# Kernel optimization log

Hardware: AMD Instinct MI355X
Metric: run time of the kernel (lower is better)

The kernel has to match this reference:

```python
import jax, jax.numpy as jnp
import numpy as np

B, T, D, H = 4, 2048, 1024, 16
HS = D // H

def _layernorm(x, g, b, eps=1e-5):
    mu = jnp.mean(x, axis=-1, keepdims=True)
    var = jnp.var(x, axis=-1, keepdims=True)
    return (x - mu) * jax.lax.rsqrt(var + eps) * g + b

def setup_inputs() -> dict:
    key = jax.random.key(0)
    ks = jax.random.split(key, 8)
    s = 0.02
    return {
        "x": jax.random.normal(ks[0], (B, T, D), jnp.float32),
        "wq": jax.random.normal(ks[1], (D, D), jnp.float32) * s,
        "wk": jax.random.normal(ks[2], (D, D), jnp.float32) * s,
        "wv": jax.random.normal(ks[3], (D, D), jnp.float32) * s,
        "wo": jax.random.normal(ks[4], (D, D), jnp.float32) * s,
        "bo": jnp.zeros((D,), jnp.float32),
        "w1": jax.random.normal(ks[5], (D, 4 * D), jnp.float32) * s,
        "b1": jnp.zeros((4 * D,), jnp.float32),
        "w2": jax.random.normal(ks[6], (4 * D, D), jnp.float32) * s,
        "b2": jnp.zeros((D,), jnp.float32),
        "g1": jnp.ones((D,), jnp.float32),
        "be1": jnp.zeros((D,), jnp.float32),
        "g2": jnp.ones((D,), jnp.float32),
        "be2": jnp.zeros((D,), jnp.float32),
    }

def reference(x, wq, wk, wv, wo, bo, w1, b1, w2, b2, g1, be1, g2, be2):
    b, t, d = x.shape
    h = H
    hs = d // h
    # --- pre-LN + multi-head causal self-attention ---
    xn = _layernorm(x, g1, be1)
    q = (xn @ wq).reshape(b, t, h, hs).transpose(0, 2, 1, 3)  # [b,h,t,hs]
    k = (xn @ wk).reshape(b, t, h, hs).transpose(0, 2, 1, 3)
    v = (xn @ wv).reshape(b, t, h, hs).transpose(0, 2, 1, 3)
    # NOTE: original scales by C**-0.5 where C = embedded_size (not head_size)
    scale = jnp.asarray(d, x.dtype) ** -0.5
    wei = jnp.einsum("bhqd,bhkd->bhqk", q, k) * scale
    causal = jnp.tril(jnp.ones((t, t), bool))
    wei = jnp.where(causal, wei, -jnp.inf)
    wei = jax.nn.softmax(wei, axis=-1)
    attn = jnp.einsum("bhqk,bhkd->bhqd", wei, v)
    attn = attn.transpose(0, 2, 1, 3).reshape(b, t, d)
    x = x + attn @ wo + bo
    # --- pre-LN + FFN ---
    xn2 = _layernorm(x, g2, be2)
    x = x + jax.nn.relu(xn2 @ w1 + b1) @ w2 + b2
    return x
```

## Files before the change

### kernel.cpp

```cpp
#include <hip/hip_runtime.h>
#include <hip/hip_bf16.h>
#include <stdint.h>

typedef __hip_bfloat16 bf16;
typedef __attribute__((ext_vector_type(8))) short bf16x8_t;
typedef __attribute__((ext_vector_type(4))) float f32x4_t;
typedef __attribute__((ext_vector_type(16))) float f32x16_t;
typedef __attribute__((ext_vector_type(2))) unsigned int u32x2_t;

#define B_ 4
#define T_ 2048
#define D_ 1024
#define H_ 16
#define HS_ 64

__device__ __forceinline__ void gload_lds16(const void* g, void* l) {
    __builtin_amdgcn_global_load_lds(
        (const __attribute__((address_space(1))) unsigned int*)g,
        (__attribute__((address_space(3))) unsigned int*)l, 16, 0, 0);
}

__device__ __forceinline__ bf16x8_t ldsv8(const bf16* p) {
    return *(const bf16x8_t*)p;
}

__device__ __forceinline__ unsigned pack2(float a, float b) {
    union { bf16 h[2]; unsigned u; } t;
    t.h[0] = __float2bfloat16(a);
    t.h[1] = __float2bfloat16(b);
    return t.u;
}

__global__ __launch_bounds__(256) void transpose_cvt(
    const float* __restrict__ W, bf16* __restrict__ WT, int K, int N)
{
    __shared__ float tile[32][33];
    const int nbx = N >> 5;
    const int bx = blockIdx.x % nbx;
    const int by = blockIdx.x / nbx;
    const int n0 = bx << 5, k0 = by << 5;
    const int tx = threadIdx.x & 31, ty = threadIdx.x >> 5;
#pragma unroll
    for (int i = 0; i < 32; i += 8)
        tile[ty + i][tx] = W[(long)(k0 + ty + i) * N + n0 + tx];
    __syncthreads();
#pragma unroll
    for (int i = 0; i < 32; i += 8)
        WT[(long)(n0 + ty + i) * K + k0 + tx] = __float2bfloat16(tile[tx][ty + i]);
}

__global__ __launch_bounds__(256) void vhead_transpose(
    const bf16* __restrict__ V, bf16* __restrict__ VT)
{
    __shared__ bf16 tile[32][33];
    int idx = blockIdx.x;
    const int tt  = idx & 63;   idx >>= 6;
    const int hst = idx & 1;    idx >>= 1;
    const int bh  = idx;
    const int b = bh >> 4, h = bh & 15;
    const int tx = threadIdx.x & 31, ty = threadIdx.x >> 5;
    const long vrow = (long)b * T_ + tt * 32;
    const int  vcol = h * HS_ + hst * 32;
#pragma unroll
    for (int i = 0; i < 32; i += 8)
        tile[ty + i][tx] = V[(vrow + ty + i) * D_ + vcol + tx];
    __syncthreads();
    const long orow = (long)bh * HS_ + hst * 32;
#pragma unroll
    for (int i = 0; i < 32; i += 8)
        VT[(orow + ty + i) * T_ + tt * 32 + tx] = tile[tx][ty + i];
}

__global__ __launch_bounds__(256) void ln_k(
    const float* __restrict__ x, const float* __restrict__ g,
    const float* __restrict__ be, bf16* __restrict__ out)
{
    const long row = blockIdx.x;
    const int t = threadIdx.x;
    const float4 v = ((const float4*)(x + row * D_))[t];
    float s  = v.x + v.y + v.z + v.w;
    float s2 = v.x * v.x + v.y * v.y + v.z * v.z + v.w * v.w;
#pragma unroll
    for (int m = 1; m < 64; m <<= 1) {
        s  += __shfl_xor(s, m, 64);
        s2 += __shfl_xor(s2, m, 64);
    }
    __shared__ float red[8];
    const int wv = t >> 6, ln = t & 63;
    if (ln == 0) { red[wv] = s; red[4 + wv] = s2; }
    __syncthreads();
    s  = red[0] + red[1] + red[2] + red[3];
    s2 = red[4] + red[5] + red[6] + red[7];
    const float mu  = s * (1.f / (float)D_);
    const float var = s2 * (1.f / (float)D_) - mu * mu;
    const float rs  = rsqrtf(var + 1e-5f);
    const float4 gv = ((const float4*)g)[t];
    const float4 bv = ((const float4*)be)[t];
    union { bf16 h[4]; short4 s4; } u;
    u.h[0] = __float2bfloat16((v.x - mu) * rs * gv.x + bv.x);
    u.h[1] = __float2bfloat16((v.y - mu) * rs * gv.y + bv.y);
    u.h[2] = __float2bfloat16((v.z - mu) * rs * gv.z + bv.z);
    u.h[3] = __float2bfloat16((v.w - mu) * rs * gv.w + bv.w);
    ((short4*)(out + row * D_))[t] = u.s4;
}

template<int HAS_BIAS, int RELU, int HAS_RES, int OUT_BF16>
__global__ __launch_bounds__(256, 2) void gemm_bt(
    const bf16* __restrict__ A, const bf16* __restrict__ BT,
    const float* __restrict__ bias, const float* __restrict__ res,
    void* __restrict__ Cout, int M, int N, int K)
{
    __shared__ bf16 As[128 * 32];
    __shared__ bf16 Bs[128 * 32];
    const int tid  = threadIdx.x;
    const int wave = tid >> 6;
    const int lane = tid & 63;
    const int nbn  = N >> 7;
    const int bm = blockIdx.x / nbn;
    const int bn = blockIdx.x % nbn;
    const int row0 = bm << 7, col0 = bn << 7;
    const int wm = wave & 1, wn = wave >> 1;

    const int srow = tid >> 2;
    const int scol = (tid & 3) << 3;
    const bf16* aSrc = A  + (long)(row0 + srow) * K + scol;
    const bf16* bSrc = BT + (long)(col0 + srow) * K + scol;
    bf16* aDst1 = As + wave * 512;
    bf16* aDst2 = As + 2048 + wave * 512;
    bf16* bDst1 = Bs + wave * 512;
    bf16* bDst2 = Bs + 2048 + wave * 512;

    f32x4_t acc[4][4] = {};

    const int fr = lane & 15;
    const int fk = (lane >> 4) << 3;

    for (int k0 = 0; k0 < K; k0 += 32) {
        gload_lds16(aSrc + k0, aDst1);
        gload_lds16(aSrc + k0 + (long)64 * K, aDst2);
        gload_lds16(bSrc + k0, bDst1);
        gload_lds16(bSrc + k0 + (long)64 * K, bDst2);
        __syncthreads();
        bf16x8_t a[4], b[4];
#pragma unroll
        for (int m = 0; m < 4; ++m)
            a[m] = ldsv8(As + (wm * 64 + m * 16 + fr) * 32 + fk);
#pragma unroll
        for (int n = 0; n < 4; ++n)
            b[n] = ldsv8(Bs + (wn * 64 + n * 16 + fr) * 32 + fk);
#pragma unroll
        for (int m = 0; m < 4; ++m)
#pragma unroll
            for (int n = 0; n < 4; ++n)
                acc[m][n] = __builtin_amdgcn_mfma_f32_16x16x32_bf16(a[m], b[n], acc[m][n], 0, 0, 0);
        __syncthreads();
    }

    const int orow = (lane >> 4) << 2;
#pragma unroll
    for (int m = 0; m < 4; ++m) {
        const int rbase = row0 + wm * 64 + m * 16 + orow;
#pragma unroll
        for (int n = 0; n < 4; ++n) {
            const int c = col0 + wn * 64 + n * 16 + fr;
            float bv = 0.f;
            if (HAS_BIAS) bv = bias[c];
#pragma unroll
            for (int r = 0; r < 4; ++r) {
                float v = acc[m][n][r] + bv;
                if (RELU) v = fmaxf(v, 0.f);
                if (HAS_RES) v += res[(long)(rbase + r) * N + c];
                if (OUT_BF16)
                    ((bf16*)Cout)[(long)(rbase + r) * N + c] = __float2bfloat16(v);
                else
                    ((float*)Cout)[(long)(rbase + r) * N + c] = v;
            }
        }
    }
}

__global__ __launch_bounds__(512, 4) void attn_flash(
    const bf16* __restrict__ Q, const bf16* __restrict__ Kg,
    const bf16* __restrict__ VT, bf16* __restrict__ O)
{
    __shared__ bf16 Ks[2][64 * 64];
    __shared__ bf16 Vs[2][64 * 64];

    const int tid = threadIdx.x;
    const int w   = tid >> 6;
    const int ln  = tid & 63;
    const int l31 = ln & 31;
    const int hi  = ln >> 5;
    const int hi8 = hi << 3;

    const int qb = 7 - (int)blockIdx.x;
    const int bh = blockIdx.y;
    const long rowBase = (long)(bh >> 4) * T_;
    const int colBase = (bh & 15) * HS_;

    const int qwbase = qb * 256 + w * 32;
    const int qabs   = qwbase + l31;
    const int ctb  = qb * 4 + 3;
    const int ct_w = qb * 4 + (w >> 1);

    const bf16* qp = Q + (rowBase + qabs) * D_ + colBase + hi8;
    bf16x8_t qf[4];
#pragma unroll
    for (int s = 0; s < 4; ++s) qf[s] = *(const bf16x8_t*)(qp + 16 * s);

    f32x16_t oA = {}, oB = {};
    float mOld = -1e30f, lSum = 0.f;
    const float kE = 0.0450842200278f;

    const int srow = tid >> 3;
    const int schunk = (((tid & 7) ^ (srow & 7)) << 3);
    const bf16* kSrc = Kg + (rowBase + srow) * D_ + colBase + schunk;
    const bf16* vSrc = VT + ((long)bh * HS_ + srow) * T_ + schunk;

    gload_lds16(kSrc, &Ks[0][w * 512]);
    gload_lds16(vSrc, &Vs[0][w * 512]);

    for (int c = 0; c <= ctb; ++c) {
        const int cur = c & 1;
        __syncthreads();

        if (c < ctb) {
            gload_lds16(kSrc + (long)(c + 1) * 64 * D_, &Ks[cur ^ 1][w * 512]);
            gload_lds16(vSrc + (c + 1) * 64, &Vs[cur ^ 1][w * 512]);
        }
        if (c > ct_w) continue;

        const bf16* K_ = Ks[cur];
        const bf16* V_ = Vs[cur];
        const int swzk = (l31 & 7) << 3;

        for (int st = 0; st < 2; ++st) {
            if (c * 64 + st * 32 > qwbase + 31) break;

            f32x16_t sa = {};
            const int krow = st * 32 + l31;
#pragma unroll
            for (int s = 0; s < 4; ++s) {
                bf16x8_t kf = ldsv8(K_ + krow * 64 + ((16 * s + hi8) ^ swzk));
                sa = __builtin_amdgcn_mfma_f32_32x32x16_bf16(kf, qf[s], sa, 0, 0, 0);
            }

            if (c == ct_w) {
                const int kb0 = c * 64 + st * 32 + 4 * hi;
#pragma unroll
                for (int r = 0; r < 16; ++r) {
                    const int kabs = kb0 + (r & 3) + 8 * (r >> 2);
                    if (kabs > qabs) sa[r] = -1e30f;
                }
            }

            float rm = sa[0];
#pragma unroll
            for (int r = 1; r < 16; ++r) rm = fmaxf(rm, sa[r]);
            {
                u32x2_t rr = __builtin_amdgcn_permlane32_swap(
                    __float_as_uint(rm), __float_as_uint(rm), false, false);
                rm = fmaxf(__uint_as_float(rr.x), __uint_as_float(rr.y));
            }
            const float mN = fmaxf(mOld, rm);
            const float corr = exp2f((mOld - mN) * kE);
            mOld = mN;
            const float nmk = -mN * kE;
#pragma unroll
            for (int r = 0; r < 16; ++r) sa[r] = exp2f(fmaf(sa[r], kE, nmk));
            float rs = sa[0];
#pragma unroll
            for (int r = 1; r < 16; ++r) rs += sa[r];
            {
                u32x2_t rr = __builtin_amdgcn_permlane32_swap(
                    __float_as_uint(rs), __float_as_uint(rs), false, false);
                rs = __uint_as_float(rr.x) + __uint_as_float(rr.y);
            }
            lSum = lSum * corr + rs;
#pragma unroll
            for (int r = 0; r < 16; ++r) { oA[r] *= corr; oB[r] *= corr; }

            unsigned pk_[8];
#pragma unroll
            for (int i = 0; i < 8; ++i) pk_[i] = pack2(sa[2 * i], sa[2 * i + 1]);
            union { unsigned u[4]; bf16x8_t v; } W0, W1;
            {
                u32x2_t ra = __builtin_amdgcn_permlane32_swap(pk_[0], pk_[2], false, false);
                u32x2_t rb = __builtin_amdgcn_permlane32_swap(pk_[1], pk_[3], false, false);
                W0.u[0] = ra.x; W0.u[1] = rb.x; W0.u[2] = ra.y; W0.u[3] = rb.y;
                u32x2_t rc = __builtin_amdgcn_permlane32_swap(pk_[4], pk_[6], false, false);
                u32x2_t rd = __builtin_amdgcn_permlane32_swap(pk_[5], pk_[7], false, false);
                W1.u[0] = rc.x; W1.u[1] = rd.x; W1.u[2] = rc.y; W1.u[3] = rd.y;
            }

#pragma unroll
            for (int m = 0; m < 2; ++m) {
                const int kcol = 16 * (st * 2 + m) + hi8;
                bf16x8_t vf0 = ldsv8(V_ + l31 * 64 + (kcol ^ swzk));
                oA = __builtin_amdgcn_mfma_f32_32x32x16_bf16(vf0, m ? W1.v : W0.v, oA, 0, 0, 0);
                const int vr1 = 32 + l31;
                bf16x8_t vf1 = ldsv8(V_ + vr1 * 64 + (kcol ^ swzk));
                oB = __builtin_amdgcn_mfma_f32_32x32x16_bf16(vf1, m ? W1.v : W0.v, oB, 0, 0, 0);
            }
        }
    }

    const float inv = 1.f / lSum;
    bf16* Op = O + (rowBase + qabs) * D_ + colBase;
#pragma unroll
    for (int g = 0; g < 4; ++g) {
        u32x2_t sA, sB;
        sA.x = pack2(oA[4 * g + 0] * inv, oA[4 * g + 1] * inv);
        sA.y = pack2(oA[4 * g + 2] * inv, oA[4 * g + 3] * inv);
        sB.x = pack2(oB[4 * g + 0] * inv, oB[4 * g + 1] * inv);
        sB.y = pack2(oB[4 * g + 2] * inv, oB[4 * g + 3] * inv);
        *(u32x2_t*)(Op + 8 * g + 4 * hi)      = sA;
        *(u32x2_t*)(Op + 32 + 8 * g + 4 * hi) = sB;
    }
}

extern "C" void kernel_launch(void* const* d_in, const int* in_sizes, int n_in,
                              void* d_out, int out_size, void* d_ws, size_t ws_size,
                              hipStream_t stream)
{
    (void)in_sizes; (void)n_in; (void)out_size; (void)ws_size;
    const float* x   = (const float*)d_in[0];
    const float* wq  = (const float*)d_in[1];
    const float* wk  = (const float*)d_in[2];
    const float* wv  = (const float*)d_in[3];
    const float* wo  = (const float*)d_in[4];
    const float* bo  = (const float*)d_in[5];
    const float* w1  = (const float*)d_in[6];
    const float* b1  = (const float*)d_in[7];
    const float* w2  = (const float*)d_in[8];
    const float* b2  = (const float*)d_in[9];
    const float* g1  = (const float*)d_in[10];
    const float* be1 = (const float*)d_in[11];
    const float* g2  = (const float*)d_in[12];
    const float* be2 = (const float*)d_in[13];
    float* out = (float*)d_out;

    char* ws = (char*)d_ws;
    const size_t SLOT = (size_t)8192 * 1024 * 2;
    bf16* xn     = (bf16*)(ws);
    bf16* attnb  = (bf16*)(ws);
    bf16* qb     = (bf16*)(ws + SLOT);
    bf16* xn2    = (bf16*)(ws + SLOT);
    bf16* kb     = (bf16*)(ws + 2 * SLOT);
    bf16* vb     = (bf16*)(ws + 3 * SLOT);
    bf16* vtb    = (bf16*)(ws + 4 * SLOT);
    bf16* hidden = (bf16*)(ws + 2 * SLOT);
    float* x1    = (float*)(ws + 6 * SLOT);
    char* wpos   = ws + 6 * SLOT + (size_t)33554432;
    bf16* wqT = (bf16*)(wpos);
    bf16* wkT = (bf16*)(wpos + (size_t)2097152);
    bf16* wvT = (bf16*)(wpos + (size_t)2 * 2097152);
    bf16* woT = (bf16*)(wpos + (size_t)3 * 2097152);
    bf16* w1T = (bf16*)(wpos + (size_t)4 * 2097152);
    bf16* w2T = (bf16*)(wpos + (size_t)4 * 2097152 + 8388608);

    transpose_cvt<<<dim3(1024), 256, 0, stream>>>(wq, wqT, 1024, 1024);
    transpose_cvt<<<dim3(1024), 256, 0, stream>>>(wk, wkT, 1024, 1024);
    transpose_cvt<<<dim3(1024), 256, 0, stream>>>(wv, wvT, 1024, 1024);
    transpose_cvt<<<dim3(1024), 256, 0, stream>>>(wo, woT, 1024, 1024);
    transpose_cvt<<<dim3(4096), 256, 0, stream>>>(w1, w1T, 1024, 4096);
    transpose_cvt<<<dim3(4096), 256, 0, stream>>>(w2, w2T, 4096, 1024);

    ln_k<<<8192, 256, 0, stream>>>(x, g1, be1, xn);

    gemm_bt<0, 0, 0, 1><<<512, 256, 0, stream>>>(xn, wqT, nullptr, nullptr, qb, 8192, 1024, 1024);
    gemm_bt<0, 0, 0, 1><<<512, 256, 0, stream>>>(xn, wkT, nullptr, nullptr, kb, 8192, 1024, 1024);
    gemm_bt<0, 0, 0, 1><<<512, 256, 0, stream>>>(xn, wvT, nullptr, nullptr, vb, 8192, 1024, 1024);

    vhead_transpose<<<8192, 256, 0, stream>>>(vb, vtb);

    attn_flash<<<dim3(8, 64), 512, 0, stream>>>(qb, kb, vtb, attnb);

    gemm_bt<1, 0, 1, 0><<<512, 256, 0, stream>>>(attnb, woT, bo, x, x1, 8192, 1024, 1024);

    ln_k<<<8192, 256, 0, stream>>>(x1, g2, be2, xn2);

    gemm_bt<1, 1, 0, 1><<<2048, 256, 0, stream>>>(xn2, w1T, b1, nullptr, hidden, 8192, 4096, 1024);

    gemm_bt<1, 0, 1, 0><<<512, 256, 0, stream>>>(hidden, w2T, b2, x1, out, 8192, 1024, 4096);
}
```

Baseline: 597.6 us.

## Fuse QKV projections, remap GEMM blocks by XCD, restructure flash attention softmax

Merges the three Q/K/V projection GEMMs into one GEMM with N=3072 over contiguous transposed weights, and updates the V-transpose and attention kernels to read from the fused QKV buffer. The GEMM block index is remapped so consecutive tiles land on the same XCD, aiming for better L2 reuse. The attention kernel now handles a full 64-key tile per iteration with one softmax pass. It also skips the output rescale when the running max grows by no more than a threshold, which cuts exp and multiply work but may risk overflow, and it lowers the occupancy hint from 4 to 2.

```diff
diff --git a/kernel.cpp b/kernel.cpp
--- a/kernel.cpp
+++ b/kernel.cpp
@@ -13,6 +13,7 @@
 #define D_ 1024
 #define H_ 16
 #define HS_ 64
+#define QKV_LD 3072
 
 __device__ __forceinline__ void gload_lds16(const void* g, void* l) {
     __builtin_amdgcn_global_load_lds(
@@ -50,7 +51,7 @@
 }
 
 __global__ __launch_bounds__(256) void vhead_transpose(
-    const bf16* __restrict__ V, bf16* __restrict__ VT)
+    const bf16* __restrict__ QKV, bf16* __restrict__ VT)
 {
     __shared__ bf16 tile[32][33];
     int idx = blockIdx.x;
@@ -60,10 +61,10 @@
     const int b = bh >> 4, h = bh & 15;
     const int tx = threadIdx.x & 31, ty = threadIdx.x >> 5;
     const long vrow = (long)b * T_ + tt * 32;
-    const int  vcol = h * HS_ + hst * 32;
+    const int  vcol = 2048 + h * HS_ + hst * 32;
 #pragma unroll
     for (int i = 0; i < 32; i += 8)
-        tile[ty + i][tx] = V[(vrow + ty + i) * D_ + vcol + tx];
+        tile[ty + i][tx] = QKV[(vrow + ty + i) * QKV_LD + vcol + tx];
     __syncthreads();
     const long orow = (long)bh * HS_ + hst * 32;
 #pragma unroll
@@ -116,8 +117,10 @@
     const int wave = tid >> 6;
     const int lane = tid & 63;
     const int nbn  = N >> 7;
-    const int bm = blockIdx.x / nbn;
-    const int bn = blockIdx.x % nbn;
+    const int cpx  = gridDim.x >> 3;
+    const int bid  = (blockIdx.x & 7) * cpx + (blockIdx.x >> 3);
+    const int bm = bid / nbn;
+    const int bn = bid % nbn;
     const int row0 = bm << 7, col0 = bn << 7;
     const int wm = wave & 1, wn = wave >> 1;
 
@@ -179,9 +182,9 @@
     }
 }
 
-__global__ __launch_bounds__(512, 4) void attn_flash(
-    const bf16* __restrict__ Q, const bf16* __restrict__ Kg,
-    const bf16* __restrict__ VT, bf16* __restrict__ O)
+__global__ __launch_bounds__(512, 2) void attn_flash(
+    const bf16* __restrict__ QKV, const bf16* __restrict__ VT,
+    bf16* __restrict__ O)
 {
     __shared__ bf16 Ks[2][64 * 64];
     __shared__ bf16 Vs[2][64 * 64];
@@ -203,103 +206,147 @@
     const int ctb  = qb * 4 + 3;
     const int ct_w = qb * 4 + (w >> 1);
 
-    const bf16* qp = Q + (rowBase + qabs) * D_ + colBase + hi8;
+    const bf16* qp = QKV + (rowBase + qabs) * QKV_LD + colBase + hi8;
     bf16x8_t qf[4];
 #pragma unroll
     for (int s = 0; s < 4; ++s) qf[s] = *(const bf16x8_t*)(qp + 16 * s);
 
     f32x16_t oA = {}, oB = {};
     float mOld = -1e30f, lSum = 0.f;
-    const float kE = 0.0450842200278f;
+    const float kE  = 0.0450842200278f;
+    const float THR = 256.0f;
 
     const int srow = tid >> 3;
     const int schunk = (((tid & 7) ^ (srow & 7)) << 3);
-    const bf16* kSrc = Kg + (rowBase + srow) * D_ + colBase + schunk;
+    const bf16* kSrc = QKV + (rowBase + srow) * QKV_LD + 1024 + colBase + schunk;
     const bf16* vSrc = VT + ((long)bh * HS_ + srow) * T_ + schunk;
 
     gload_lds16(kSrc, &Ks[0][w * 512]);
     gload_lds16(vSrc, &Vs[0][w * 512]);
+
+    const int swzk = (l31 & 7) << 3;
 
     for (int c = 0; c <= ctb; ++c) {
         const int cur = c & 1;
         __syncthreads();
 
         if (c < ctb) {
-            gload_lds16(kSrc + (long)(c + 1) * 64 * D_, &Ks[cur ^ 1][w * 512]);
+            gload_lds16(kSrc + (long)(c + 1) * 64 * QKV_LD, &Ks[cur ^ 1][w * 512]);
             gload_lds16(vSrc + (c + 1) * 64, &Vs[cur ^ 1][w * 512]);
         }
         if (c > ct_w) continue;
 
         const bf16* K_ = Ks[cur];
         const bf16* V_ = Vs[cur];
-        const int swzk = (l31 & 7) << 3;
-
-        for (int st = 0; st < 2; ++st) {
-            if (c * 64 + st * 32 > qwbase + 31) break;
-
-            f32x16_t sa = {};
-            const int krow = st * 32 + l31;
+        const bool diag = (c == ct_w);
+        const bool two  = !(diag && !(w & 1));
+
+        f32x16_t s0 = {}, s1 = {};
+#pragma unroll
+        for (int s = 0; s < 4; ++s) {
+            bf16x8_t kf = ldsv8(K_ + l31 * 64 + ((16 * s + hi8) ^ swzk));
+            s0 = __builtin_amdgcn_mfma_f32_32x32x16_bf16(kf, qf[s], s0, 0, 0, 0);
+        }
+        if (two) {
 #pragma unroll
             for (int s = 0; s < 4; ++s) {
-                bf16x8_t kf = ldsv8(K_ + krow * 64 + ((16 * s + hi8) ^ swzk));
-                sa = __builtin_amdgcn_mfma_f32_32x32x16_bf16(kf, qf[s], sa, 0, 0, 0);
+                bf16x8_t kf = ldsv8(K_ + (32 + l31) * 64 + ((16 * s + hi8) ^ swzk));
+                s1 = __builtin_amdgcn_mfma_f32_32x32x16_bf16(kf, qf[s], s1, 0, 0, 0);
             }
-
-            if (c == ct_w) {
-                const int kb0 = c * 64 + st * 32 + 4 * hi;
-#pragma unroll
-                for (int r = 0; r < 16; ++r) {
-                    const int kabs = kb0 + (r & 3) + 8 * (r >> 2);
-                    if (kabs > qabs) sa[r] = -1e30f;
-                }
+        }
+
+        if (diag) {
+            const int stm = w & 1;
+            const int kb0 = c * 64 + stm * 32 + 4 * hi;
+            if (stm) {
+#pragma unroll
+                for (int r = 0; r < 16; ++r)
+                    if (kb0 + (r & 3) + 8 * (r >> 2) > qabs) s1[r] = -1e30f;
+            } else {
+#pragma unroll
+                for (int r = 0; r < 16; ++r)
+                    if (kb0 + (r & 3) + 8 * (r >> 2) > qabs) s0[r] = -1e30f;
             }
-
-            float rm = sa[0];
-#pragma unroll
-            for (int r = 1; r < 16; ++r) rm = fmaxf(rm, sa[r]);
-            {
-                u32x2_t rr = __builtin_amdgcn_permlane32_swap(
-                    __float_as_uint(rm), __float_as_uint(rm), false, false);
-                rm = fmaxf(__uint_as_float(rr.x), __uint_as_float(rr.y));
-            }
+        }
+
+        float rm = s0[0];
+#pragma unroll
+        for (int r = 1; r < 16; ++r) rm = fmaxf(rm, s0[r]);
+        if (two) {
+#pragma unroll
+            for (int r = 0; r < 16; ++r) rm = fmaxf(rm, s1[r]);
+        }
+        {
+            u32x2_t rr = __builtin_amdgcn_permlane32_swap(
+                __float_as_uint(rm), __float_as_uint(rm), false, false);
+            rm = fmaxf(__uint_as_float(rr.x), __uint_as_float(rr.y));
+        }
+        if (!__all(rm <= mOld + THR)) {
             const float mN = fmaxf(mOld, rm);
             const float corr = exp2f((mOld - mN) * kE);
+#pragma unroll
+            for (int r = 0; r < 16; ++r) { oA[r] *= corr; oB[r] *= corr; }
+            lSum *= corr;
             mOld = mN;
-            const float nmk = -mN * kE;
-#pragma unroll
-            for (int r = 0; r < 16; ++r) sa[r] = exp2f(fmaf(sa[r], kE, nmk));
-            float rs = sa[0];
-#pragma unroll
-            for (int r = 1; r < 16; ++r) rs += sa[r];
-            {
-                u32x2_t rr = __builtin_amdgcn_permlane32_swap(
-                    __float_as_uint(rs), __float_as_uint(rs), false, false);
-                rs = __uint_as_float(rr.x) + __uint_as_float(rr.y);
-            }
-            lSum = lSum * corr + rs;
-#pragma unroll
-            for (int r = 0; r < 16; ++r) { oA[r] *= corr; oB[r] *= corr; }
-
+        }
+        const float nmk = -mOld * kE;
+#pragma unroll
+        for (int r = 0; r < 16; ++r) s0[r] = exp2f(fmaf(s0[r], kE, nmk));
+        if (two) {
+#pragma unroll
+            for (int r = 0; r < 16; ++r) s1[r] = exp2f(fmaf(s1[r], kE, nmk));
+        }
+        float rs = s0[0];
+#pragma unroll
+        for (int r = 1; r < 16; ++r) rs += s0[r];
+        if (two) {
+#pragma unroll
+            for (int r = 0; r < 16; ++r) rs += s1[r];
+        }
+        {
+            u32x2_t rr = __builtin_amdgcn_permlane32_swap(
+                __float_as_uint(rs), __float_as_uint(rs), false, false);
+            rs = __uint_as_float(rr.x) + __uint_as_float(rr.y);
+        }
+        lSum += rs;
+
+        {
             unsigned pk_[8];
 #pragma unroll
-            for (int i = 0; i < 8; ++i) pk_[i] = pack2(sa[2 * i], sa[2 * i + 1]);
+            for (int i = 0; i < 8; ++i) pk_[i] = pack2(s0[2 * i], s0[2 * i + 1]);
             union { unsigned u[4]; bf16x8_t v; } W0, W1;
-            {
-                u32x2_t ra = __builtin_amdgcn_permlane32_swap(pk_[0], pk_[2], false, false);
-                u32x2_t rb = __builtin_amdgcn_permlane32_swap(pk_[1], pk_[3], false, false);
-                W0.u[0] = ra.x; W0.u[1] = rb.x; W0.u[2] = ra.y; W0.u[3] = rb.y;
-                u32x2_t rc = __builtin_amdgcn_permlane32_swap(pk_[4], pk_[6], false, false);
-                u32x2_t rd = __builtin_amdgcn_permlane32_swap(pk_[5], pk_[7], false, false);
-                W1.u[0] = rc.x; W1.u[1] = rd.x; W1.u[2] = rc.y; W1.u[3] = rd.y;
-            }
-
+            u32x2_t ra = __builtin_amdgcn_permlane32_swap(pk_[0], pk_[2], false, false);
+            u32x2_t rb = __builtin_amdgcn_permlane32_swap(pk_[1], pk_[3], false, false);
+            W0.u[0] = ra.x; W0.u[1] = rb.x; W0.u[2] = ra.y; W0.u[3] = rb.y;
+            u32x2_t rc = __builtin_amdgcn_permlane32_swap(pk_[4], pk_[6], false, false);
+            u32x2_t rd = __builtin_amdgcn_permlane32_swap(pk_[5], pk_[7], false, false);
+            W1.u[0] = rc.x; W1.u[1] = rd.x; W1.u[2] = rc.y; W1.u[3] = rd.y;
 #pragma unroll
             for (int m = 0; m < 2; ++m) {
-                const int kcol = 16 * (st * 2 + m) + hi8;
+                const int kcol = 16 * m + hi8;
                 bf16x8_t vf0 = ldsv8(V_ + l31 * 64 + (kcol ^ swzk));
                 oA = __builtin_amdgcn_mfma_f32_32x32x16_bf16(vf0, m ? W1.v : W0.v, oA, 0, 0, 0);
-                const int vr1 = 32 + l31;
-                bf16x8_t vf1 = ldsv8(V_ + vr1 * 64 + (kcol ^ swzk));
+                bf16x8_t vf1 = ldsv8(V_ + (32 + l31) * 64 + (kcol ^ swzk));
+                oB = __builtin_amdgcn_mfma_f32_32x32x16_bf16(vf1, m ? W1.v : W0.v, oB, 0, 0, 0);
+            }
+        }
+        if (two) {
+            unsigned pk_[8];
+#pragma unroll
+            for (int i = 0; i < 8; ++i) pk_[i] = pack2(s1[2 * i], s1[2 * i + 1]);
+            union { unsigned u[4]; bf16x8_t v; } W0, W1;
+            u32x2_t ra = __builtin_amdgcn_permlane32_swap(pk_[0], pk_[2], false, false);
+            u32x2_t rb = __builtin_amdgcn_permlane32_swap(pk_[1], pk_[3], false, false);
+            W0.u[0] = ra.x; W0.u[1] = rb.x; W0.u[2] = ra.y; W0.u[3] = rb.y;
+            u32x2_t rc = __builtin_amdgcn_permlane32_swap(pk_[4], pk_[6], false, false);
+            u32x2_t rd = __builtin_amdgcn_permlane32_swap(pk_[5], pk_[7], false, false);
+            W1.u[0] = rc.x; W1.u[1] = rd.x; W1.u[2] = rc.y; W1.u[3] = rd.y;
+#pragma unroll
+            for (int m = 0; m < 2; ++m) {
+                const int kcol = 16 * (2 + m) + hi8;
+                bf16x8_t vf0 = ldsv8(V_ + l31 * 64 + (kcol ^ swzk));
+                oA = __builtin_amdgcn_mfma_f32_32x32x16_bf16(vf0, m ? W1.v : W0.v, oA, 0, 0, 0);
+                bf16x8_t vf1 = ldsv8(V_ + (32 + l31) * 64 + (kcol ^ swzk));
                 oB = __builtin_amdgcn_mfma_f32_32x32x16_bf16(vf1, m ? W1.v : W0.v, oB, 0, 0, 0);
             }
         }
@@ -344,14 +391,13 @@
     const size_t SLOT = (size_t)8192 * 1024 * 2;
     bf16* xn     = (bf16*)(ws);
     bf16* attnb  = (bf16*)(ws);
-    bf16* qb     = (bf16*)(ws + SLOT);
+    bf16* qkv    = (bf16*)(ws + SLOT);
     bf16* xn2    = (bf16*)(ws + SLOT);
-    bf16* kb     = (bf16*)(ws + 2 * SLOT);
-    bf16* vb     = (bf16*)(ws + 3 * SLOT);
     bf16* vtb    = (bf16*)(ws + 4 * SLOT);
     bf16* hidden = (bf16*)(ws + 2 * SLOT);
     float* x1    = (float*)(ws + 6 * SLOT);
     char* wpos   = ws + 6 * SLOT + (size_t)33554432;
+    bf16* wqkvT = (bf16*)(wpos);
     bf16* wqT = (bf16*)(wpos);
     bf16* wkT = (bf16*)(wpos + (size_t)2097152);
     bf16* wvT = (bf16*)(wpos + (size_t)2 * 2097152);
@@ -368,13 +414,11 @@
 
     ln_k<<<8192, 256, 0, stream>>>(x, g1, be1, xn);
 
-    gemm_bt<0, 0, 0, 1><<<512, 256, 0, stream>>>(xn, wqT, nullptr, nullptr, qb, 8192, 1024, 1024);
-    gemm_bt<0, 0, 0, 1><<<512, 256, 0, stream>>>(xn, wkT, nullptr, nullptr, kb, 8192, 1024, 1024);
-    gemm_bt<0, 0, 0, 1><<<512, 256, 0, stream>>>(xn, wvT, nullptr, nullptr, vb, 8192, 1024, 1024);
-
-    vhead_transpose<<<8192, 256, 0, stream>>>(vb, vtb);
-
-    attn_flash<<<dim3(8, 64), 512, 0, stream>>>(qb, kb, vtb, attnb);
+    gemm_bt<0, 0, 0, 1><<<1536, 256, 0, stream>>>(xn, wqkvT, nullptr, nullptr, qkv, 8192, 3072, 1024);
+
+    vhead_transpose<<<8192, 256, 0, stream>>>(qkv, vtb);
+
+    attn_flash<<<dim3(8, 64), 512, 0, stream>>>(qkv, vtb, attnb);
 
     gemm_bt<1, 0, 1, 0><<<512, 256, 0, stream>>>(attnb, woT, bo, x, x1, 8192, 1024, 1024);
 
```

Measured after the change: 561.0 us. 1.07x faster.
